# Performance work log

Measured on AMD Instinct MI355X. Metric: run time of the kernel, lower is better.

## Reference

```python
import jax, jax.numpy as jnp
import numpy as np

N, D, E, L, NL = 100000, 64, 400000, 4, 10000
NEG = jnp.float32(-1e30)


def _make_graph(key):
    k1, k2, k3, k4 = jax.random.split(key, 4)
    ncov = N - NL
    # nodes [0, NL) never appear as source -> exactly NL leaves
    src_cov = jnp.arange(ncov, dtype=jnp.int32) + NL
    src_rand = jax.random.randint(k1, (E - ncov,), NL, N, dtype=jnp.int32)
    src = jnp.concatenate([src_cov, src_rand])
    dst = jax.random.randint(k2, (E,), 0, N, dtype=jnp.int32)
    edge_index = jnp.stack([src, dst])  # [2, E]
    edge_attr = jax.random.normal(k3, (E, D), jnp.float32)
    # partition edges into L 'topological level' masks
    edge_masks = (jnp.arange(E) % L)[None, :] == jnp.arange(L)[:, None]  # [L, E] bool
    x = jax.random.normal(k4, (N, D), jnp.float32)
    return x, edge_index, edge_attr, edge_masks


def setup_inputs() -> dict:
    key = jax.random.key(0)
    kg1, kg2, kp = jax.random.split(key, 3)
    x1, ei1, ea1, em1 = _make_graph(kg1)
    x2, ei2, ea2, em2 = _make_graph(kg2)
    ks = jax.random.split(kp, 10)
    s = 1.0 / np.sqrt(D)
    params = {
        'We': jax.random.normal(ks[0], (D, D), jnp.float32) * s,
        'be': jax.random.normal(ks[1], (D,), jnp.float32) * s,
        'Wa': jax.random.normal(ks[2], (1, 2 * D), jnp.float32) * s,
        'ba': jax.random.normal(ks[3], (1,), jnp.float32) * s,
        'Wih': jax.random.normal(ks[4], (3 * D, D), jnp.float32) * s,
        'Whh': jax.random.normal(ks[5], (3 * D, D), jnp.float32) * s,
        'bih': jax.random.normal(ks[6], (3 * D,), jnp.float32) * s,
        'bhh': jax.random.normal(ks[7], (3 * D,), jnp.float32) * s,
        'Wc': jax.random.normal(ks[8], (2 * D, 2 * D), jnp.float32) * s,
        'bc': jax.random.normal(ks[9], (2 * D,), jnp.float32) * s,
    }
    return dict(x1=x1, edge_index1=ei1, edge_attr1=ea1, edge_masks1=em1,
                x2=x2, edge_index2=ei2, edge_attr2=ea2, edge_masks2=em2,
                **params, n_leaf=NL)


def _gru(x, h, Wih, Whh, bih, bhh):
    # torch.nn.GRUCell math
    gi = x @ Wih.T + bih
    gh = h @ Whh.T + bhh
    ir, iz, in_ = jnp.split(gi, 3, axis=-1)
    hr, hz, hn = jnp.split(gh, 3, axis=-1)
    r = jax.nn.sigmoid(ir + hr)
    z = jax.nn.sigmoid(iz + hz)
    n = jnp.tanh(in_ + r * hn)
    return (1.0 - z) * n + z * h


def _flow_forward(x, edge_index, edge_attr, edge_masks,
                  We, be, Wa, ba, Wih, Whh, bih, bhh):
    Nn, Dm = x.shape
    src, dst = edge_index[0], edge_index[1]
    root = jnp.ones((Nn,), bool).at[dst].set(False)  # nodes with no incoming edge
    eemb = edge_attr @ We.T + be                     # [E, D] edge_lin
    # roots: GRU with zero hidden; others start at 0 (zeros_like in torch)
    h0 = jnp.where(root[:, None], _gru(x, jnp.zeros_like(x), Wih, Whh, bih, bhh), 0.0)
    q = x[dst]                                       # h_prev_i, level-invariant

    def step(h, mask):
        k = h[src] + eemb                            # h_j + edge_emb
        logit = (jnp.concatenate([q, k], axis=-1) @ Wa.T + ba)[:, 0]  # [E]
        ml = jnp.where(mask, logit, NEG)
        mx = jnp.maximum(jax.ops.segment_max(ml, dst, num_segments=Nn), NEG)
        ex = jnp.where(mask, jnp.exp(ml - mx[dst]), 0.0)  # scatter-softmax numerator
        den = jax.ops.segment_sum(ex, dst, num_segments=Nn)
        alpha = ex / (den[dst] + 1e-16)
        msg = jax.ops.segment_sum(alpha[:, None] * h[src], dst, num_segments=Nn)
        nm = jax.ops.segment_sum(mask.astype(jnp.float32), dst, num_segments=Nn) > 0
        h_new = _gru(x, msg, Wih, Whh, bih, bhh)     # input=h_prev, hidden=msg
        return jnp.where(nm[:, None], h_new, h), None

    h, _ = jax.lax.scan(step, h0, edge_masks)
    return h


def reference(x1, edge_index1, edge_attr1, edge_masks1,
              x2, edge_index2, edge_attr2, edge_masks2,
              We, be, Wa, ba, Wih, Whh, bih, bhh, Wc, bc, n_leaf):
    o1 = _flow_forward(x1, edge_index1, edge_attr1, edge_masks1,
                       We, be, Wa, ba, Wih, Whh, bih, bhh)
    o2 = _flow_forward(x2, edge_index2, edge_attr2, edge_masks2,
                       We, be, Wa, ba, Wih, Whh, bih, bhh)
    Dm = x1.shape[1]
    leaf1 = jnp.ones((x1.shape[0],), bool).at[edge_index1[0]].set(False)
    leaf2 = jnp.ones((x2.shape[0],), bool).at[edge_index2[0]].set(False)
    idx1 = jnp.nonzero(leaf1, size=n_leaf)[0]
    idx2 = jnp.nonzero(leaf2, size=n_leaf)[0]
    feat = jnp.concatenate([o1[idx1], o2[idx2]], axis=-1) @ Wc.T + bc  # [NL, 2D]
    o1 = o1.at[idx1].set(feat[:, :Dm])
    o2 = o2.at[idx2].set(feat[:, Dm:])
    return (o1, o2)
```

## Files before the change

### kernel.cpp

```cpp
#include <hip/hip_runtime.h>

#define NN 100000
#define DD 64
#define EE 400000
#define LL 4
#define NLEAF 10000
#define NT (2*NN)
#define ETOT (2*EE)
#define M4 (4*NT)
#define NBLK ((M4 + 1023)/1024)

typedef __attribute__((ext_vector_type(8))) short bf8v;
typedef __attribute__((ext_vector_type(4))) float f4v;

__device__ __forceinline__ float rcp_(float x){ return __builtin_amdgcn_rcpf(x); }
__device__ __forceinline__ float sigm_(float x){ return rcp_(1.f + __expf(-x)); }
__device__ __forceinline__ float tanh_(float x){
  x = fminf(fmaxf(x, -15.f), 15.f);
  float a = __expf(2.f*x);
  return (a - 1.f) * rcp_(a + 1.f);
}
__device__ __forceinline__ float wave_sum(float p){
  #pragma unroll
  for (int m = 1; m < 64; m <<= 1) p += __shfl_xor(p, m, 64);
  return p;
}
__device__ __forceinline__ unsigned short f2b(float f){
  union { float f; unsigned int u; } v; v.f = f;
  unsigned int r = v.u + 0x7FFF + ((v.u >> 16) & 1);
  return (unsigned short)(r >> 16);
}
__device__ __forceinline__ float b2f(unsigned short b){
  union { unsigned int u; float f; } v; v.u = ((unsigned int)b) << 16;
  return v.f;
}
__device__ __forceinline__ int cnt_at(const unsigned int* pcnt, int i){
  int l = i / NT; int td = i - l*NT;
  return (int)((pcnt[td] >> (8*l)) & 255u);
}

__global__ void k_init(unsigned int* __restrict__ pcnt,
                       int* __restrict__ wlcnt, int* __restrict__ row_ptr,
                       float* __restrict__ hdot,
                       float* __restrict__ vvec, float* __restrict__ c0v,
                       unsigned short* __restrict__ whh_bf,
                       unsigned short* __restrict__ wih_bf,
                       unsigned short* __restrict__ hbf,
                       const float* __restrict__ We, const float* __restrict__ Wa,
                       const float* __restrict__ be, const float* __restrict__ Whh,
                       const float* __restrict__ Wih) {
  int tid = blockIdx.x*blockDim.x + threadIdx.x;
  int stride = gridDim.x*blockDim.x;
  for (int i = tid; i < NT; i += stride) { pcnt[i] = 0u; hdot[i] = 0.f; }
  for (int i = tid; i < 192*64; i += stride) whh_bf[i] = f2b(Whh[i]);
  for (int i = tid; i < 208*64; i += stride) {
    int n = i >> 6, k = i & 63;
    unsigned short v;
    if (n < 192)       v = f2b(Wih[i]);
    else if (n == 192) v = f2b(Wa[k]);
    else               v = 0;
    wih_bf[i] = v;
  }
  uint4 z4 = make_uint4(0,0,0,0);
  uint4* hz = (uint4*)hbf;
  for (int i = tid; i < NT*8; i += stride) hz[i] = z4;
  if (blockIdx.x == 0 && threadIdx.x < 64) {
    int c = threadIdx.x;
    float acc = 0.f;
    for (int d = 0; d < 64; ++d) acc += We[d*64 + c] * Wa[64 + d];
    vvec[c] = acc;
    float p = wave_sum(be[c] * Wa[64 + c]);
    if (c == 0) { c0v[0] = p; row_ptr[M4] = ETOT; }
    if (c < 8) wlcnt[c] = 0;
  }
}

__global__ void k_edot(const float* __restrict__ ea1, const float* __restrict__ ea2,
                       const int* __restrict__ ei1, const int* __restrict__ ei2,
                       const float* __restrict__ vvec, const float* __restrict__ c0v,
                       float* __restrict__ edot, unsigned int* __restrict__ pcnt) {
  int tid = blockIdx.x*blockDim.x + threadIdx.x;
  int stride = gridDim.x*blockDim.x;
  for (int ee = tid; ee < ETOT; ee += stride) {
    int g = ee >= EE;
    int e = ee - g*EE;
    const int* ei = g ? ei2 : ei1;
    int d = ei[EE + e];
    atomicAdd(&pcnt[g*NN + d], 1u << (8*(e & 3)));
  }
  int lane = threadIdx.x & 63;
  int wave = blockIdx.x*(blockDim.x>>6) + (threadIdx.x>>6);
  int nw = gridDim.x*(blockDim.x>>6);
  int grp = lane >> 4, l16 = lane & 15;
  float4 v4 = ((const float4*)vvec)[l16];
  float c0 = c0v[0];
  const int NIT = ETOT/16;
  int it = wave;
  float4 c0_, c1_, c2_, c3_;
  if (it < NIT) {
    int e0 = it*16 + grp; int g = e0 >= EE;
    const float* ea = g ? ea2 : ea1; long eb = e0 - g*EE;
    c0_ = ((const float4*)(ea + eb*64))[l16];
    c1_ = ((const float4*)(ea + (eb+4)*64))[l16];
    c2_ = ((const float4*)(ea + (eb+8)*64))[l16];
    c3_ = ((const float4*)(ea + (eb+12)*64))[l16];
  }
  while (it < NIT) {
    int jt = it + nw;
    float4 n0, n1, n2, n3;
    if (jt < NIT) {
      int e0 = jt*16 + grp; int g = e0 >= EE;
      const float* ea = g ? ea2 : ea1; long eb = e0 - g*EE;
      n0 = ((const float4*)(ea + eb*64))[l16];
      n1 = ((const float4*)(ea + (eb+4)*64))[l16];
      n2 = ((const float4*)(ea + (eb+8)*64))[l16];
      n3 = ((const float4*)(ea + (eb+12)*64))[l16];
    } else {
      n0 = n1 = n2 = n3 = make_float4(0.f,0.f,0.f,0.f);
    }
    float p0 = c0_.x*v4.x + c0_.y*v4.y + c0_.z*v4.z + c0_.w*v4.w;
    float p1 = c1_.x*v4.x + c1_.y*v4.y + c1_.z*v4.z + c1_.w*v4.w;
    float p2 = c2_.x*v4.x + c2_.y*v4.y + c2_.z*v4.z + c2_.w*v4.w;
    float p3 = c3_.x*v4.x + c3_.y*v4.y + c3_.z*v4.z + c3_.w*v4.w;
    #pragma unroll
    for (int m = 1; m < 16; m <<= 1) {
      p0 += __shfl_xor(p0, m, 64); p1 += __shfl_xor(p1, m, 64);
      p2 += __shfl_xor(p2, m, 64); p3 += __shfl_xor(p3, m, 64);
    }
    if (l16 == 0) {
      int e0 = it*16 + grp;
      edot[e0]      = p0 + c0;
      edot[e0 +  4] = p1 + c0;
      edot[e0 +  8] = p2 + c0;
      edot[e0 + 12] = p3 + c0;
    }
    c0_ = n0; c1_ = n1; c2_ = n2; c3_ = n3;
    it = jt;
  }
}

__global__ __launch_bounds__(256) void k_scan1(const unsigned int* __restrict__ pcnt,
                                               int* __restrict__ row_ptr,
                                               int* __restrict__ partials) {
  __shared__ int ts[256];
  int tx = threadIdx.x;
  int base = blockIdx.x*1024 + tx*4;
  int v[4]; int s = 0;
  #pragma unroll
  for (int u = 0; u < 4; ++u) { v[u] = (base+u < M4) ? cnt_at(pcnt, base+u) : 0; s += v[u]; }
  ts[tx] = s; __syncthreads();
  for (int off = 1; off < 256; off <<= 1) {
    int t = (tx >= off) ? ts[tx-off] : 0;
    __syncthreads();
    ts[tx] += t;
    __syncthreads();
  }
  int excl = ts[tx] - s;
  #pragma unroll
  for (int u = 0; u < 4; ++u) {
    if (base+u < M4) row_ptr[base+u] = excl;
    excl += v[u];
  }
  if (tx == 255) partials[blockIdx.x] = ts[255];
}

__global__ __launch_bounds__(256) void k_scan2(int* __restrict__ partials) {
  __shared__ int ts[256];
  int tx = threadIdx.x;
  int carry = 0;
  for (int base = 0; base < NBLK; base += 256) {
    int i = base + tx;
    int v = (i < NBLK) ? partials[i] : 0;
    ts[tx] = v; __syncthreads();
    for (int off = 1; off < 256; off <<= 1) {
      int t = (tx >= off) ? ts[tx-off] : 0;
      __syncthreads();
      ts[tx] += t;
      __syncthreads();
    }
    int incl = ts[tx];
    int tot = ts[255];
    __syncthreads();
    if (i < NBLK) partials[i] = incl - v + carry;
    carry += tot;
  }
}

__global__ __launch_bounds__(256) void k_scan3(int* __restrict__ row_ptr,
                                               const int* __restrict__ partials,
                                               const unsigned int* __restrict__ pcnt,
                                               int* __restrict__ wl, int* __restrict__ wlcnt,
                                               int* __restrict__ lastlvl) {
  int tdl = blockIdx.x*blockDim.x + threadIdx.x;
  if (tdl < NT) {
    unsigned pv = pcnt[tdl];
    int ll = -1;
    if      (pv & 0xFF000000u) ll = 3;
    else if (pv & 0x00FF0000u) ll = 2;
    else if (pv & 0x0000FF00u) ll = 1;
    else if (pv & 0x000000FFu) ll = 0;
    lastlvl[tdl] = ll;
  }
  __shared__ int cnt4[4];
  __shared__ int base4[4];
  int tx = threadIdx.x;
  if (tx < 4) cnt4[tx] = 0;
  __syncthreads();
  int base = blockIdx.x*1024 + tx*4;
  int add = partials[blockIdx.x];
  int rank[4]; int lvl[4]; bool val[4];
  #pragma unroll
  for (int u = 0; u < 4; ++u) {
    int i = base + u;
    val[u] = false;
    if (i < M4) {
      row_ptr[i] += add;
      if (cnt_at(pcnt, i) > 0) {
        int l = i / NT;
        lvl[u] = l;
        rank[u] = atomicAdd(&cnt4[l], 1);
        val[u] = true;
      }
    }
  }
  __syncthreads();
  if (tx < 4 && cnt4[tx] > 0) base4[tx] = atomicAdd(&wlcnt[tx], cnt4[tx]);
  __syncthreads();
  #pragma unroll
  for (int u = 0; u < 4; ++u) {
    if (val[u]) {
      int l = lvl[u];
      wl[l*NT + base4[l] + rank[u]] = (base + u) - l*NT;
    }
  }
}

__global__ __launch_bounds__(256) void k_fillgix(
    const int* __restrict__ ei1, const int* __restrict__ ei2,
    const float* __restrict__ edot, const float* __restrict__ ba,
    const int* __restrict__ row_ptr, unsigned int* __restrict__ pcnt,
    int2* __restrict__ csr,
    const float* __restrict__ x1, const float* __restrict__ x2,
    const unsigned short* __restrict__ wih_bf,
    const float* __restrict__ bih, const float* __restrict__ bhh,
    const float* __restrict__ Wa, const int* __restrict__ lastlvl,
    ushort2* __restrict__ gi01, unsigned short* __restrict__ gi2p,
    float* __restrict__ xdot, float* __restrict__ hdot,
    float* __restrict__ hout, unsigned short* __restrict__ hbf) {
  {
    int tid = blockIdx.x*blockDim.x + threadIdx.x;
    int stride = gridDim.x*blockDim.x;
    float bav = ba[0];
    for (int ee = tid; ee < ETOT; ee += stride) {
      int g = ee >= EE;
      int e = ee - g*EE;
      const int* ei = g ? ei2 : ei1;
      int s = ei[e], d = ei[EE + e];
      int l = e & 3;
      int td = g*NN + d;
      unsigned old = atomicAdd(&pcnt[td], (unsigned)(0u - (1u << (8*l))));
      int slot = (int)((old >> (8*l)) & 255u) - 1;
      int pos = row_ptr[l*NT + td] + slot;
      csr[pos] = make_int2(g*NN + s, __float_as_int(edot[ee] + bav));
    }
  }
  int lane = threadIdx.x & 63, w = threadIdx.x >> 6;
  int l15 = lane & 15, quad = lane >> 4;
  int wave = blockIdx.x*4 + w, nw = gridDim.x*4;
  float bi0[4],bi1[4],bi2[4],bh0[4],bh1[4],bh2[4],wk4[4];
  #pragma unroll
  for (int tt = 0; tt < 4; ++tt) {
    int f = l15 + 16*tt;
    bi0[tt]=bih[f]; bi1[tt]=bih[64+f]; bi2[tt]=bih[128+f];
    bh0[tt]=bhh[f]; bh1[tt]=bhh[64+f]; bh2[tt]=bhh[128+f];
    wk4[tt]=Wa[64+f];
  }
  for (int tl = wave; tl < NT/16; tl += nw) {
    int ta = tl*16 + l15;
    const float* xp = (ta < NN) ? x1 + (size_t)ta*64 : x2 + (size_t)(ta-NN)*64;
    float4 v0 = ((const float4*)xp)[quad*2];
    float4 v1 = ((const float4*)xp)[quad*2 + 1];
    float4 v2 = ((const float4*)xp)[quad*2 + 8];
    float4 v3 = ((const float4*)xp)[quad*2 + 9];
    bf8v a0, a1;
    a0[0]=(short)f2b(v0.x); a0[1]=(short)f2b(v0.y); a0[2]=(short)f2b(v0.z); a0[3]=(short)f2b(v0.w);
    a0[4]=(short)f2b(v1.x); a0[5]=(short)f2b(v1.y); a0[6]=(short)f2b(v1.z); a0[7]=(short)f2b(v1.w);
    a1[0]=(short)f2b(v2.x); a1[1]=(short)f2b(v2.y); a1[2]=(short)f2b(v2.z); a1[3]=(short)f2b(v2.w);
    a1[4]=(short)f2b(v3.x); a1[5]=(short)f2b(v3.y); a1[6]=(short)f2b(v3.z); a1[7]=(short)f2b(v3.w);
    int rt[4];
    #pragma unroll
    for (int r = 0; r < 4; ++r) rt[r] = (lastlvl[tl*16 + quad*4 + r] < 0);
    float hds[4] = {0.f, 0.f, 0.f, 0.f};
    #pragma unroll
    for (int tt = 0; tt < 4; ++tt) {
      bf8v bR0 = *(const bf8v*)&wih_bf[((tt  )*16 + l15)*64 + quad*8];
      bf8v bR1 = *(const bf8v*)&wih_bf[((tt  )*16 + l15)*64 + 32 + quad*8];
      bf8v bZ0 = *(const bf8v*)&wih_bf[((tt+4)*16 + l15)*64 + quad*8];
      bf8v bZ1 = *(const bf8v*)&wih_bf[((tt+4)*16 + l15)*64 + 32 + quad*8];
      bf8v bN0 = *(const bf8v*)&wih_bf[((tt+8)*16 + l15)*64 + quad*8];
      bf8v bN1 = *(const bf8v*)&wih_bf[((tt+8)*16 + l15)*64 + 32 + quad*8];
      f4v zR = {0.f,0.f,0.f,0.f}, zZ = {0.f,0.f,0.f,0.f}, zN = {0.f,0.f,0.f,0.f};
      zR = __builtin_amdgcn_mfma_f32_16x16x32_bf16(a0, bR0, zR, 0, 0, 0);
      zR = __builtin_amdgcn_mfma_f32_16x16x32_bf16(a1, bR1, zR, 0, 0, 0);
      zZ = __builtin_amdgcn_mfma_f32_16x16x32_bf16(a0, bZ0, zZ, 0, 0, 0);
      zZ = __builtin_amdgcn_mfma_f32_16x16x32_bf16(a1, bZ1, zZ, 0, 0, 0);
      zN = __builtin_amdgcn_mfma_f32_16x16x32_bf16(a0, bN0, zN, 0, 0, 0);
      zN = __builtin_amdgcn_mfma_f32_16x16x32_bf16(a1, bN1, zN, 0, 0, 0);
      int f = tt*16 + l15;
      #pragma unroll
      for (int r = 0; r < 4; ++r) {
        int t = tl*16 + quad*4 + r;
        float g0 = zR[r] + bi0[tt];
        float g1 = zZ[r] + bi1[tt];
        float g2 = zN[r] + bi2[tt];
        ushort2 p; p.x = f2b(g0); p.y = f2b(g1);
        gi01[(size_t)t*64 + f] = p;
        gi2p[(size_t)t*64 + f] = f2b(g2);
        if (rt[r]) {
          float rr = sigm_(g0 + bh0[tt]);
          float zz = sigm_(g1 + bh1[tt]);
          float nn = tanh_(g2 + rr*bh2[tt]);
          float hv = (1.f - zz)*nn;
          hout[(size_t)t*64 + f] = hv;
          hbf[(size_t)t*64 + f] = f2b(hv);
          hds[r] += hv * wk4[tt];
        }
      }
    }
    bf8v bx0 = *(const bf8v*)&wih_bf[(192 + l15)*64 + quad*8];
    bf8v bx1 = *(const bf8v*)&wih_bf[(192 + l15)*64 + 32 + quad*8];
    f4v zX = {0.f,0.f,0.f,0.f};
    zX = __builtin_amdgcn_mfma_f32_16x16x32_bf16(a0, bx0, zX, 0, 0, 0);
    zX = __builtin_amdgcn_mfma_f32_16x16x32_bf16(a1, bx1, zX, 0, 0, 0);
    #pragma unroll
    for (int r = 0; r < 4; ++r) {
      int t = tl*16 + quad*4 + r;
      if (l15 == 0) xdot[t] = zX[r];
      if (rt[r]) {
        float h = hds[r];
        h += __shfl_xor(h, 1, 64); h += __shfl_xor(h, 2, 64);
        h += __shfl_xor(h, 4, 64); h += __shfl_xor(h, 8, 64);
        if (l15 == 0) hdot[t] = h;
      }
    }
  }
}

__global__ void k_msg(const int* __restrict__ row_ptr, const int2* __restrict__ csr,
                      const float* __restrict__ xdot,
                      const float* __restrict__ hdot, const unsigned short* __restrict__ hbf,
                      const int* __restrict__ wl, const int* __restrict__ wlcnt,
                      int level, unsigned short* __restrict__ msgn_bf) {
  int l16 = threadIdx.x & 15;
  int grp = (blockIdx.x*blockDim.x + threadIdx.x) >> 4;
  int ngrp = (gridDim.x*blockDim.x) >> 4;
  int cnt = wlcnt[level];
  for (int i = grp; i < cnt; i += ngrp) {
    int t = wl[level*NT + i];
    int bi = level*NT + t;
    int p0 = row_ptr[bi], p1 = row_ptr[bi+1];
    float xd = xdot[t];
    float den = 0.f;
    float m0 = 0.f, m1 = 0.f, m2 = 0.f, m3 = 0.f;
    for (int p = p0; p < p1; ++p) {
      int2 pr = csr[p];
      int s = pr.x;
      float wv = __expf(xd + hdot[s] + __int_as_float(pr.y));
      den += wv;
      ushort4 hv = *(const ushort4*)(hbf + (size_t)s*64 + l16*4);
      m0 += wv*b2f(hv.x); m1 += wv*b2f(hv.y); m2 += wv*b2f(hv.z); m3 += wv*b2f(hv.w);
    }
    float rd = rcp_(den + 1e-16f);
    ushort4 o;
    o.x = f2b(m0*rd); o.y = f2b(m1*rd); o.z = f2b(m2*rd); o.w = f2b(m3*rd);
    *(ushort4*)(msgn_bf + (long)i*64 + l16*4) = o;
  }
}

__global__ __launch_bounds__(256) void k_gru(
    const unsigned short* __restrict__ whh_bf, const float* __restrict__ bhh,
    const float* __restrict__ Wa,
    const ushort2* __restrict__ gi01, const unsigned short* __restrict__ gi2p,
    const int* __restrict__ wl, const int* __restrict__ wlcnt,
    const int* __restrict__ lastlvl, int level,
    const unsigned short* __restrict__ msgn_bf,
    float* __restrict__ hout, unsigned short* __restrict__ hbf,
    float* __restrict__ hdot) {
  int lane = threadIdx.x & 63, w = threadIdx.x >> 6;
  int l15 = lane & 15, quad = lane >> 4;
  int cnt = wlcnt[level];
  int ntile = (cnt + 15) >> 4;
  int wave = blockIdx.x*4 + w, nw = gridDim.x*4;
  float bh0[4], bh1[4], bh2[4], wk4[4];
  #pragma unroll
  for (int tt = 0; tt < 4; ++tt) {
    int f = tt*16 + l15;
    bh0[tt]=bhh[f]; bh1[tt]=bhh[64+f]; bh2[tt]=bhh[128+f];
    wk4[tt]=Wa[64+f];
  }
  for (int tl = wave; tl < ntile; tl += nw) {
    int base = tl*16;
    long abase = (long)(base + l15)*64;
    bf8v a0 = *(const bf8v*)&msgn_bf[abase + quad*8];
    bf8v a1 = *(const bf8v*)&msgn_bf[abase + 32 + quad*8];
    f4v acc[12];
    #pragma unroll
    for (int nt = 0; nt < 12; ++nt) {
      bf8v b0 = *(const bf8v*)&whh_bf[(nt*16 + l15)*64 + quad*8];
      bf8v b1 = *(const bf8v*)&whh_bf[(nt*16 + l15)*64 + 32 + quad*8];
      f4v z = {0.f, 0.f, 0.f, 0.f};
      z = __builtin_amdgcn_mfma_f32_16x16x32_bf16(a0, b0, z, 0, 0, 0);
      acc[nt] = __builtin_amdgcn_mfma_f32_16x16x32_bf16(a1, b1, z, 0, 0, 0);
    }
    #pragma unroll
    for (int r = 0; r < 4; ++r) {
      int i = base + quad*4 + r;
      if (i < cnt) {
        int t = wl[level*NT + i];
        int ll = lastlvl[t];
        float hds = 0.f;
        #pragma unroll
        for (int tt = 0; tt < 4; ++tt) {
          int f = tt*16 + l15;
          ushort2 p01 = gi01[(size_t)t*64 + f];
          float g2v = b2f(gi2p[(size_t)t*64 + f]);
          float mv  = b2f(msgn_bf[(long)i*64 + f]);
          float rr = sigm_(b2f(p01.x) + acc[tt][r]   + bh0[tt]);
          float zz = sigm_(b2f(p01.y) + acc[tt+4][r] + bh1[tt]);
          float nn = tanh_(g2v + rr*(acc[tt+8][r] + bh2[tt]));
          float hv = (1.f - zz)*nn + zz*mv;
          if (ll == level) hout[(size_t)t*64 + f] = hv;
          if (level < 3)  hbf[(size_t)t*64 + f] = f2b(hv);
          hds += hv * wk4[tt];
        }
        if (level < 3) {
          hds += __shfl_xor(hds, 1, 64);
          hds += __shfl_xor(hds, 2, 64);
          hds += __shfl_xor(hds, 4, 64);
          hds += __shfl_xor(hds, 8, 64);
          if (l15 == 0) hdot[t] = hds;
        }
      }
    }
  }
}

__global__ __launch_bounds__(256) void k_final(const float* __restrict__ Wc,
                                               const float* __restrict__ bc,
                                               float* __restrict__ hout) {
  __shared__ float WT[128*128];
  for (int idx = threadIdx.x; idx < 128*128; idx += 256) {
    int j = idx >> 7, c = idx & 127;
    WT[c*128 + j] = Wc[idx];
  }
  __syncthreads();
  int lane = threadIdx.x & 63, w = threadIdx.x >> 6;
  int wave = blockIdx.x*4 + w, nw = gridDim.x*4;
  float bc0 = bc[lane], bc1 = bc[64 + lane];
  for (int i = wave; i < NLEAF; i += nw) {
    float h1v = hout[(long)i*64 + lane];
    float h2v = hout[(long)(NN + i)*64 + lane];
    float acc0 = 0.f, acc1 = 0.f;
    for (int c = 0; c < 64; ++c) {
      float m1 = __shfl(h1v, c, 64);
      float m2 = __shfl(h2v, c, 64);
      acc0 += WT[c*128 + lane]      * m1 + WT[(64+c)*128 + lane]      * m2;
      acc1 += WT[c*128 + 64 + lane] * m1 + WT[(64+c)*128 + 64 + lane] * m2;
    }
    hout[(long)i*64 + lane]        = acc0 + bc0;
    hout[(long)(NN + i)*64 + lane] = acc1 + bc1;
  }
}

extern "C" void kernel_launch(void* const* d_in, const int* in_sizes, int n_in,
                              void* d_out, int out_size, void* d_ws, size_t ws_size,
                              hipStream_t stream) {
  const float* x1  = (const float*)d_in[0];
  const int*   ei1 = (const int*)  d_in[1];
  const float* ea1 = (const float*)d_in[2];
  const float* x2  = (const float*)d_in[4];
  const int*   ei2 = (const int*)  d_in[5];
  const float* ea2 = (const float*)d_in[6];
  const float* We  = (const float*)d_in[8];
  const float* be  = (const float*)d_in[9];
  const float* Wa  = (const float*)d_in[10];
  const float* ba  = (const float*)d_in[11];
  const float* Wih = (const float*)d_in[12];
  const float* Whh = (const float*)d_in[13];
  const float* bih = (const float*)d_in[14];
  const float* bhh = (const float*)d_in[15];
  const float* Wc  = (const float*)d_in[16];
  const float* bc  = (const float*)d_in[17];
  float* hout = (float*)d_out;

  float* f = (float*)d_ws;
  ushort2* gi01 = (ushort2*)f;        f += (size_t)NT*64;
  unsigned short* gi2p    = (unsigned short*)f;  f += (size_t)NT*32;
  unsigned short* msgn_bf = (unsigned short*)f;  f += (size_t)NT*32;
  unsigned short* hbf     = (unsigned short*)f;  f += (size_t)NT*32;
  unsigned short* whh_bf  = (unsigned short*)f;  f += 8192;
  unsigned short* wih_bf  = (unsigned short*)f;  f += 8192;
  float* edot = f;  f += ETOT;
  float* xdot = f;  f += NT;
  float* hdot = f;  f += NT;
  float* vvec = f;  f += 64;
  float* c0v  = f;  f += 64;
  int2* csr     = (int2*)f; f += (size_t)2*ETOT;
  unsigned int* pcnt = (unsigned int*)f;  f += NT;
  int* row_ptr  = (int*)f;  f += (M4 + 64);
  int* lastlvl  = (int*)f;  f += NT;
  int* wl       = (int*)f;  f += 4*NT;
  int* wlcnt    = (int*)f;  f += 64;
  int* partials = (int*)f;  f += 1024;

  k_init <<<dim3(1024), dim3(256), 0, stream>>>(pcnt, wlcnt, row_ptr, hdot, vvec, c0v, whh_bf, wih_bf, hbf, We, Wa, be, Whh, Wih);
  k_edot <<<dim3(2048), dim3(256), 0, stream>>>(ea1, ea2, ei1, ei2, vvec, c0v, edot, pcnt);
  k_scan1<<<dim3(NBLK), dim3(256), 0, stream>>>(pcnt, row_ptr, partials);
  k_scan2<<<dim3(1),    dim3(256), 0, stream>>>(partials);
  k_scan3<<<dim3(NBLK), dim3(256), 0, stream>>>(row_ptr, partials, pcnt, wl, wlcnt, lastlvl);
  k_fillgix<<<dim3(2048), dim3(256), 0, stream>>>(ei1, ei2, edot, ba, row_ptr, pcnt, csr, x1, x2, wih_bf, bih, bhh, Wa, lastlvl, gi01, gi2p, xdot, hdot, hout, hbf);
  for (int l = 0; l < 4; ++l) {
    k_msg<<<dim3(8192), dim3(256), 0, stream>>>(row_ptr, csr, xdot, hdot, hbf, wl, wlcnt, l, msgn_bf);
    k_gru<<<dim3(2048), dim3(256), 0, stream>>>(whh_bf, bhh, Wa, gi01, gi2p, wl, wlcnt, lastlvl, l, msgn_bf, hout, hbf, hdot);
  }
  k_final<<<dim3(640), dim3(256), 0, stream>>>(Wc, bc, hout);
}
```

Before: 560.4 us.

## Fuse edge-attention dot into CSR fill and batch input-gate MFMAs

Removes the separate k_edot kernel. The per-edge projection of edge_attr onto the attention vector is now computed inside k_fillgix, right where each CSR entry is written, so the intermediate edot buffer is never stored and reloaded. The destination-count atomics move into k_init, and a small k_zero kernel now clears the counters beforehand. The input-gate MFMA loop is reorganised to issue all 13 tile products first and then run the elementwise GRU epilogue, which gives more independent MFMA work per wave but holds more accumulator registers. The explicit next-iteration prefetch of edge_attr that k_edot used is dropped.

```diff
diff --git a/kernel.cpp b/kernel.cpp
--- a/kernel.cpp
+++ b/kernel.cpp
@@ -39,19 +39,27 @@
   return (int)((pcnt[td] >> (8*l)) & 255u);
 }
 
+__global__ void k_zero(unsigned int* __restrict__ pcnt, int* __restrict__ wlcnt) {
+  int tid = blockIdx.x*blockDim.x + threadIdx.x;
+  int stride = gridDim.x*blockDim.x;
+  for (int i = tid; i < NT; i += stride) pcnt[i] = 0u;
+  if (tid < 8) wlcnt[tid] = 0;
+}
+
 __global__ void k_init(unsigned int* __restrict__ pcnt,
-                       int* __restrict__ wlcnt, int* __restrict__ row_ptr,
+                       int* __restrict__ row_ptr,
                        float* __restrict__ hdot,
                        float* __restrict__ vvec, float* __restrict__ c0v,
                        unsigned short* __restrict__ whh_bf,
                        unsigned short* __restrict__ wih_bf,
                        unsigned short* __restrict__ hbf,
+                       const int* __restrict__ ei1, const int* __restrict__ ei2,
                        const float* __restrict__ We, const float* __restrict__ Wa,
                        const float* __restrict__ be, const float* __restrict__ Whh,
                        const float* __restrict__ Wih) {
   int tid = blockIdx.x*blockDim.x + threadIdx.x;
   int stride = gridDim.x*blockDim.x;
-  for (int i = tid; i < NT; i += stride) { pcnt[i] = 0u; hdot[i] = 0.f; }
+  for (int i = tid; i < NT; i += stride) hdot[i] = 0.f;
   for (int i = tid; i < 192*64; i += stride) whh_bf[i] = f2b(Whh[i]);
   for (int i = tid; i < 208*64; i += stride) {
     int n = i >> 6, k = i & 63;
@@ -71,71 +79,13 @@
     vvec[c] = acc;
     float p = wave_sum(be[c] * Wa[64 + c]);
     if (c == 0) { c0v[0] = p; row_ptr[M4] = ETOT; }
-    if (c < 8) wlcnt[c] = 0;
-  }
-}
-
-__global__ void k_edot(const float* __restrict__ ea1, const float* __restrict__ ea2,
-                       const int* __restrict__ ei1, const int* __restrict__ ei2,
-                       const float* __restrict__ vvec, const float* __restrict__ c0v,
-                       float* __restrict__ edot, unsigned int* __restrict__ pcnt) {
-  int tid = blockIdx.x*blockDim.x + threadIdx.x;
-  int stride = gridDim.x*blockDim.x;
+  }
   for (int ee = tid; ee < ETOT; ee += stride) {
     int g = ee >= EE;
     int e = ee - g*EE;
     const int* ei = g ? ei2 : ei1;
     int d = ei[EE + e];
     atomicAdd(&pcnt[g*NN + d], 1u << (8*(e & 3)));
-  }
-  int lane = threadIdx.x & 63;
-  int wave = blockIdx.x*(blockDim.x>>6) + (threadIdx.x>>6);
-  int nw = gridDim.x*(blockDim.x>>6);
-  int grp = lane >> 4, l16 = lane & 15;
-  float4 v4 = ((const float4*)vvec)[l16];
-  float c0 = c0v[0];
-  const int NIT = ETOT/16;
-  int it = wave;
-  float4 c0_, c1_, c2_, c3_;
-  if (it < NIT) {
-    int e0 = it*16 + grp; int g = e0 >= EE;
-    const float* ea = g ? ea2 : ea1; long eb = e0 - g*EE;
-    c0_ = ((const float4*)(ea + eb*64))[l16];
-    c1_ = ((const float4*)(ea + (eb+4)*64))[l16];
-    c2_ = ((const float4*)(ea + (eb+8)*64))[l16];
-    c3_ = ((const float4*)(ea + (eb+12)*64))[l16];
-  }
-  while (it < NIT) {
-    int jt = it + nw;
-    float4 n0, n1, n2, n3;
-    if (jt < NIT) {
-      int e0 = jt*16 + grp; int g = e0 >= EE;
-      const float* ea = g ? ea2 : ea1; long eb = e0 - g*EE;
-      n0 = ((const float4*)(ea + eb*64))[l16];
-      n1 = ((const float4*)(ea + (eb+4)*64))[l16];
-      n2 = ((const float4*)(ea + (eb+8)*64))[l16];
-      n3 = ((const float4*)(ea + (eb+12)*64))[l16];
-    } else {
-      n0 = n1 = n2 = n3 = make_float4(0.f,0.f,0.f,0.f);
-    }
-    float p0 = c0_.x*v4.x + c0_.y*v4.y + c0_.z*v4.z + c0_.w*v4.w;
-    float p1 = c1_.x*v4.x + c1_.y*v4.y + c1_.z*v4.z + c1_.w*v4.w;
-    float p2 = c2_.x*v4.x + c2_.y*v4.y + c2_.z*v4.z + c2_.w*v4.w;
-    float p3 = c3_.x*v4.x + c3_.y*v4.y + c3_.z*v4.z + c3_.w*v4.w;
-    #pragma unroll
-    for (int m = 1; m < 16; m <<= 1) {
-      p0 += __shfl_xor(p0, m, 64); p1 += __shfl_xor(p1, m, 64);
-      p2 += __shfl_xor(p2, m, 64); p3 += __shfl_xor(p3, m, 64);
-    }
-    if (l16 == 0) {
-      int e0 = it*16 + grp;
-      edot[e0]      = p0 + c0;
-      edot[e0 +  4] = p1 + c0;
-      edot[e0 +  8] = p2 + c0;
-      edot[e0 + 12] = p3 + c0;
-    }
-    c0_ = n0; c1_ = n1; c2_ = n2; c3_ = n3;
-    it = jt;
   }
 }
 
@@ -236,8 +186,10 @@
 }
 
 __global__ __launch_bounds__(256) void k_fillgix(
+    const float* __restrict__ ea1, const float* __restrict__ ea2,
     const int* __restrict__ ei1, const int* __restrict__ ei2,
-    const float* __restrict__ edot, const float* __restrict__ ba,
+    const float* __restrict__ vvec, const float* __restrict__ c0v,
+    const float* __restrict__ ba,
     const int* __restrict__ row_ptr, unsigned int* __restrict__ pcnt,
     int2* __restrict__ csr,
     const float* __restrict__ x1, const float* __restrict__ x2,
@@ -247,25 +199,45 @@
     ushort2* __restrict__ gi01, unsigned short* __restrict__ gi2p,
     float* __restrict__ xdot, float* __restrict__ hdot,
     float* __restrict__ hout, unsigned short* __restrict__ hbf) {
-  {
-    int tid = blockIdx.x*blockDim.x + threadIdx.x;
-    int stride = gridDim.x*blockDim.x;
-    float bav = ba[0];
-    for (int ee = tid; ee < ETOT; ee += stride) {
-      int g = ee >= EE;
-      int e = ee - g*EE;
-      const int* ei = g ? ei2 : ei1;
-      int s = ei[e], d = ei[EE + e];
-      int l = e & 3;
-      int td = g*NN + d;
-      unsigned old = atomicAdd(&pcnt[td], (unsigned)(0u - (1u << (8*l))));
-      int slot = (int)((old >> (8*l)) & 255u) - 1;
-      int pos = row_ptr[l*NT + td] + slot;
-      csr[pos] = make_int2(g*NN + s, __float_as_int(edot[ee] + bav));
-    }
-  }
   int lane = threadIdx.x & 63, w = threadIdx.x >> 6;
   int l15 = lane & 15, quad = lane >> 4;
+  {
+    int wave = blockIdx.x*(blockDim.x>>6) + (threadIdx.x>>6);
+    int nw = gridDim.x*(blockDim.x>>6);
+    int grp = quad, l16 = l15;
+    float4 v4 = ((const float4*)vvec)[l16];
+    float cb = c0v[0] + ba[0];
+    for (int it = wave; it < ETOT/16; it += nw) {
+      int e0 = it*16 + grp;
+      int g = e0 >= EE;
+      const float* ea = g ? ea2 : ea1;
+      const int* ei = g ? ei2 : ei1;
+      long eb = e0 - g*EE;
+      float4 a0 = ((const float4*)(ea + (eb     )*64))[l16];
+      float4 a1 = ((const float4*)(ea + (eb +  4)*64))[l16];
+      float4 a2 = ((const float4*)(ea + (eb +  8)*64))[l16];
+      float4 a3 = ((const float4*)(ea + (eb + 12)*64))[l16];
+      float p0 = a0.x*v4.x + a0.y*v4.y + a0.z*v4.z + a0.w*v4.w;
+      float p1 = a1.x*v4.x + a1.y*v4.y + a1.z*v4.z + a1.w*v4.w;
+      float p2 = a2.x*v4.x + a2.y*v4.y + a2.z*v4.z + a2.w*v4.w;
+      float p3 = a3.x*v4.x + a3.y*v4.y + a3.z*v4.z + a3.w*v4.w;
+      #pragma unroll
+      for (int m = 1; m < 16; m <<= 1) {
+        p0 += __shfl_xor(p0, m, 64); p1 += __shfl_xor(p1, m, 64);
+        p2 += __shfl_xor(p2, m, 64); p3 += __shfl_xor(p3, m, 64);
+      }
+      if (l16 < 4) {
+        float pj = (l16 == 0) ? p0 : (l16 == 1) ? p1 : (l16 == 2) ? p2 : p3;
+        int e = (int)eb + 4*l16;
+        int s = ei[e], d = ei[EE + e];
+        int td = g*NN + d;
+        unsigned old = atomicAdd(&pcnt[td], (unsigned)(0u - (1u << (8*grp))));
+        int slot = (int)((old >> (8*grp)) & 255u) - 1;
+        int pos = row_ptr[grp*NT + td] + slot;
+        csr[pos] = make_int2(g*NN + s, __float_as_int(pj + cb));
+      }
+    }
+  }
   int wave = blockIdx.x*4 + w, nw = gridDim.x*4;
   float bi0[4],bi1[4],bi2[4],bh0[4],bh1[4],bh2[4],wk4[4];
   #pragma unroll
@@ -291,28 +263,24 @@
     #pragma unroll
     for (int r = 0; r < 4; ++r) rt[r] = (lastlvl[tl*16 + quad*4 + r] < 0);
     float hds[4] = {0.f, 0.f, 0.f, 0.f};
+    f4v acc[13];
     #pragma unroll
-    for (int tt = 0; tt < 4; ++tt) {
-      bf8v bR0 = *(const bf8v*)&wih_bf[((tt  )*16 + l15)*64 + quad*8];
-      bf8v bR1 = *(const bf8v*)&wih_bf[((tt  )*16 + l15)*64 + 32 + quad*8];
-      bf8v bZ0 = *(const bf8v*)&wih_bf[((tt+4)*16 + l15)*64 + quad*8];
-      bf8v bZ1 = *(const bf8v*)&wih_bf[((tt+4)*16 + l15)*64 + 32 + quad*8];
-      bf8v bN0 = *(const bf8v*)&wih_bf[((tt+8)*16 + l15)*64 + quad*8];
-      bf8v bN1 = *(const bf8v*)&wih_bf[((tt+8)*16 + l15)*64 + 32 + quad*8];
-      f4v zR = {0.f,0.f,0.f,0.f}, zZ = {0.f,0.f,0.f,0.f}, zN = {0.f,0.f,0.f,0.f};
-      zR = __builtin_amdgcn_mfma_f32_16x16x32_bf16(a0, bR0, zR, 0, 0, 0);
-      zR = __builtin_amdgcn_mfma_f32_16x16x32_bf16(a1, bR1, zR, 0, 0, 0);
-      zZ = __builtin_amdgcn_mfma_f32_16x16x32_bf16(a0, bZ0, zZ, 0, 0, 0);
-      zZ = __builtin_amdgcn_mfma_f32_16x16x32_bf16(a1, bZ1, zZ, 0, 0, 0);
-      zN = __builtin_amdgcn_mfma_f32_16x16x32_bf16(a0, bN0, zN, 0, 0, 0);
-      zN = __builtin_amdgcn_mfma_f32_16x16x32_bf16(a1, bN1, zN, 0, 0, 0);
-      int f = tt*16 + l15;
+    for (int nt = 0; nt < 13; ++nt) {
+      bf8v b0 = *(const bf8v*)&wih_bf[(nt*16 + l15)*64 + quad*8];
+      bf8v b1 = *(const bf8v*)&wih_bf[(nt*16 + l15)*64 + 32 + quad*8];
+      f4v z = {0.f, 0.f, 0.f, 0.f};
+      z = __builtin_amdgcn_mfma_f32_16x16x32_bf16(a0, b0, z, 0, 0, 0);
+      acc[nt] = __builtin_amdgcn_mfma_f32_16x16x32_bf16(a1, b1, z, 0, 0, 0);
+    }
+    #pragma unroll
+    for (int r = 0; r < 4; ++r) {
+      int t = tl*16 + quad*4 + r;
       #pragma unroll
-      for (int r = 0; r < 4; ++r) {
-        int t = tl*16 + quad*4 + r;
-        float g0 = zR[r] + bi0[tt];
-        float g1 = zZ[r] + bi1[tt];
-        float g2 = zN[r] + bi2[tt];
+      for (int tt = 0; tt < 4; ++tt) {
+        int f = tt*16 + l15;
+        float g0 = acc[tt][r]   + bi0[tt];
+        float g1 = acc[tt+4][r] + bi1[tt];
+        float g2 = acc[tt+8][r] + bi2[tt];
         ushort2 p; p.x = f2b(g0); p.y = f2b(g1);
         gi01[(size_t)t*64 + f] = p;
         gi2p[(size_t)t*64 + f] = f2b(g2);
@@ -326,16 +294,7 @@
           hds[r] += hv * wk4[tt];
         }
       }
-    }
-    bf8v bx0 = *(const bf8v*)&wih_bf[(192 + l15)*64 + quad*8];
-    bf8v bx1 = *(const bf8v*)&wih_bf[(192 + l15)*64 + 32 + quad*8];
-    f4v zX = {0.f,0.f,0.f,0.f};
-    zX = __builtin_amdgcn_mfma_f32_16x16x32_bf16(a0, bx0, zX, 0, 0, 0);
-    zX = __builtin_amdgcn_mfma_f32_16x16x32_bf16(a1, bx1, zX, 0, 0, 0);
-    #pragma unroll
-    for (int r = 0; r < 4; ++r) {
-      int t = tl*16 + quad*4 + r;
-      if (l15 == 0) xdot[t] = zX[r];
+      if (l15 == 0) xdot[t] = acc[12][r];
       if (rt[r]) {
         float h = hds[r];
         h += __shfl_xor(h, 1, 64); h += __shfl_xor(h, 2, 64);
@@ -500,7 +459,6 @@
   unsigned short* hbf     = (unsigned short*)f;  f += (size_t)NT*32;
   unsigned short* whh_bf  = (unsigned short*)f;  f += 8192;
   unsigned short* wih_bf  = (unsigned short*)f;  f += 8192;
-  float* edot = f;  f += ETOT;
   float* xdot = f;  f += NT;
   float* hdot = f;  f += NT;
   float* vvec = f;  f += 64;
@@ -513,12 +471,12 @@
   int* wlcnt    = (int*)f;  f += 64;
   int* partials = (int*)f;  f += 1024;
 
-  k_init <<<dim3(1024), dim3(256), 0, stream>>>(pcnt, wlcnt, row_ptr, hdot, vvec, c0v, whh_bf, wih_bf, hbf, We, Wa, be, Whh, Wih);
-  k_edot <<<dim3(2048), dim3(256), 0, stream>>>(ea1, ea2, ei1, ei2, vvec, c0v, edot, pcnt);
+  k_zero <<<dim3(256),  dim3(256), 0, stream>>>(pcnt, wlcnt);
+  k_init <<<dim3(1024), dim3(256), 0, stream>>>(pcnt, row_ptr, hdot, vvec, c0v, whh_bf, wih_bf, hbf, ei1, ei2, We, Wa, be, Whh, Wih);
   k_scan1<<<dim3(NBLK), dim3(256), 0, stream>>>(pcnt, row_ptr, partials);
   k_scan2<<<dim3(1),    dim3(256), 0, stream>>>(partials);
   k_scan3<<<dim3(NBLK), dim3(256), 0, stream>>>(row_ptr, partials, pcnt, wl, wlcnt, lastlvl);
-  k_fillgix<<<dim3(2048), dim3(256), 0, stream>>>(ei1, ei2, edot, ba, row_ptr, pcnt, csr, x1, x2, wih_bf, bih, bhh, Wa, lastlvl, gi01, gi2p, xdot, hdot, hout, hbf);
+  k_fillgix<<<dim3(2048), dim3(256), 0, stream>>>(ea1, ea2, ei1, ei2, vvec, c0v, ba, row_ptr, pcnt, csr, x1, x2, wih_bf, bih, bhh, Wa, lastlvl, gi01, gi2p, xdot, hdot, hout, hbf);
   for (int l = 0; l < 4; ++l) {
     k_msg<<<dim3(8192), dim3(256), 0, stream>>>(row_ptr, csr, xdot, hdot, hbf, wl, wlcnt, l, msgn_bf);
     k_gru<<<dim3(2048), dim3(256), 0, stream>>>(whh_bf, bhh, Wa, gi01, gi2p, wl, wlcnt, lastlvl, l, msgn_bf, hout, hbf, hdot);
```

Result: slower. 623.0 us (+11.2%).

## Split root GRU init into worklist kernel and restructure edge-dot loop

Applied to the files above, without the earlier changes.

Root-node (no incoming edge) initial hidden-state computation moves out of k_fillgix into a new k_roots kernel, driven by a fifth worklist built in k_scan3. This removes per-row branching and extra register pressure from the MFMA gi projection kernel, which now gets a launch_bounds occupancy hint. k_edot now does its dot-product pass first, processing two edge tiles per iteration instead of using register double-buffering, and runs the pcnt atomics afterwards. The pcnt/wlcnt zeroing moves to a separate small kernel. The cost is two extra kernel launches and re-reading gi values from global memory for root nodes.

```diff
diff --git a/kernel.cpp b/kernel.cpp
--- a/kernel.cpp
+++ b/kernel.cpp
@@ -39,8 +39,14 @@
   return (int)((pcnt[td] >> (8*l)) & 255u);
 }
 
-__global__ void k_init(unsigned int* __restrict__ pcnt,
-                       int* __restrict__ wlcnt, int* __restrict__ row_ptr,
+__global__ void k_zero(unsigned int* __restrict__ pcnt, int* __restrict__ wlcnt) {
+  int tid = blockIdx.x*blockDim.x + threadIdx.x;
+  int stride = gridDim.x*blockDim.x;
+  for (int i = tid; i < NT; i += stride) pcnt[i] = 0u;
+  if (tid < 8) wlcnt[tid] = 0;
+}
+
+__global__ void k_init(int* __restrict__ row_ptr,
                        float* __restrict__ hdot,
                        float* __restrict__ vvec, float* __restrict__ c0v,
                        unsigned short* __restrict__ whh_bf,
@@ -51,7 +57,7 @@
                        const float* __restrict__ Wih) {
   int tid = blockIdx.x*blockDim.x + threadIdx.x;
   int stride = gridDim.x*blockDim.x;
-  for (int i = tid; i < NT; i += stride) { pcnt[i] = 0u; hdot[i] = 0.f; }
+  for (int i = tid; i < NT; i += stride) hdot[i] = 0.f;
   for (int i = tid; i < 192*64; i += stride) whh_bf[i] = f2b(Whh[i]);
   for (int i = tid; i < 208*64; i += stride) {
     int n = i >> 6, k = i & 63;
@@ -71,14 +77,73 @@
     vvec[c] = acc;
     float p = wave_sum(be[c] * Wa[64 + c]);
     if (c == 0) { c0v[0] = p; row_ptr[M4] = ETOT; }
-    if (c < 8) wlcnt[c] = 0;
-  }
-}
-
-__global__ void k_edot(const float* __restrict__ ea1, const float* __restrict__ ea2,
-                       const int* __restrict__ ei1, const int* __restrict__ ei2,
-                       const float* __restrict__ vvec, const float* __restrict__ c0v,
-                       float* __restrict__ edot, unsigned int* __restrict__ pcnt) {
+  }
+}
+
+__global__ __launch_bounds__(256) void k_edot(
+    const float* __restrict__ ea1, const float* __restrict__ ea2,
+    const int* __restrict__ ei1, const int* __restrict__ ei2,
+    const float* __restrict__ vvec, const float* __restrict__ c0v,
+    float* __restrict__ edot, unsigned int* __restrict__ pcnt) {
+  int lane = threadIdx.x & 63;
+  int wave = blockIdx.x*(blockDim.x>>6) + (threadIdx.x>>6);
+  int nw = gridDim.x*(blockDim.x>>6);
+  int grp = lane >> 4, l16 = lane & 15;
+  float4 v4 = ((const float4*)vvec)[l16];
+  float c0 = c0v[0];
+  const int NIT = ETOT/16;
+  for (int it = wave; it < NIT; it += 2*nw) {
+    int it2 = it + nw;
+    bool hasB = (it2 < NIT);
+    int e0 = it*16 + grp;
+    int g = e0 >= EE;
+    const float* ea = g ? ea2 : ea1;
+    long eb = e0 - (long)g*EE;
+    float4 a0 = ((const float4*)(ea + (eb     )*64))[l16];
+    float4 a1 = ((const float4*)(ea + (eb +  4)*64))[l16];
+    float4 a2 = ((const float4*)(ea + (eb +  8)*64))[l16];
+    float4 a3 = ((const float4*)(ea + (eb + 12)*64))[l16];
+    float4 b0, b1, b2, b3; int e1 = 0;
+    if (hasB) {
+      e1 = it2*16 + grp;
+      int g2 = e1 >= EE;
+      const float* eb2 = g2 ? ea2 : ea1;
+      long ebb = e1 - (long)g2*EE;
+      b0 = ((const float4*)(eb2 + (ebb     )*64))[l16];
+      b1 = ((const float4*)(eb2 + (ebb +  4)*64))[l16];
+      b2 = ((const float4*)(eb2 + (ebb +  8)*64))[l16];
+      b3 = ((const float4*)(eb2 + (ebb + 12)*64))[l16];
+    } else {
+      b0 = b1 = b2 = b3 = make_float4(0.f,0.f,0.f,0.f);
+    }
+    float p0 = a0.x*v4.x + a0.y*v4.y + a0.z*v4.z + a0.w*v4.w;
+    float p1 = a1.x*v4.x + a1.y*v4.y + a1.z*v4.z + a1.w*v4.w;
+    float p2 = a2.x*v4.x + a2.y*v4.y + a2.z*v4.z + a2.w*v4.w;
+    float p3 = a3.x*v4.x + a3.y*v4.y + a3.z*v4.z + a3.w*v4.w;
+    float q0 = b0.x*v4.x + b0.y*v4.y + b0.z*v4.z + b0.w*v4.w;
+    float q1 = b1.x*v4.x + b1.y*v4.y + b1.z*v4.z + b1.w*v4.w;
+    float q2 = b2.x*v4.x + b2.y*v4.y + b2.z*v4.z + b2.w*v4.w;
+    float q3 = b3.x*v4.x + b3.y*v4.y + b3.z*v4.z + b3.w*v4.w;
+    #pragma unroll
+    for (int m = 1; m < 16; m <<= 1) {
+      p0 += __shfl_xor(p0, m, 64); p1 += __shfl_xor(p1, m, 64);
+      p2 += __shfl_xor(p2, m, 64); p3 += __shfl_xor(p3, m, 64);
+      q0 += __shfl_xor(q0, m, 64); q1 += __shfl_xor(q1, m, 64);
+      q2 += __shfl_xor(q2, m, 64); q3 += __shfl_xor(q3, m, 64);
+    }
+    if (l16 == 0) {
+      edot[e0]      = p0 + c0;
+      edot[e0 +  4] = p1 + c0;
+      edot[e0 +  8] = p2 + c0;
+      edot[e0 + 12] = p3 + c0;
+      if (hasB) {
+        edot[e1]      = q0 + c0;
+        edot[e1 +  4] = q1 + c0;
+        edot[e1 +  8] = q2 + c0;
+        edot[e1 + 12] = q3 + c0;
+      }
+    }
+  }
   int tid = blockIdx.x*blockDim.x + threadIdx.x;
   int stride = gridDim.x*blockDim.x;
   for (int ee = tid; ee < ETOT; ee += stride) {
@@ -87,55 +152,6 @@
     const int* ei = g ? ei2 : ei1;
     int d = ei[EE + e];
     atomicAdd(&pcnt[g*NN + d], 1u << (8*(e & 3)));
-  }
-  int lane = threadIdx.x & 63;
-  int wave = blockIdx.x*(blockDim.x>>6) + (threadIdx.x>>6);
-  int nw = gridDim.x*(blockDim.x>>6);
-  int grp = lane >> 4, l16 = lane & 15;
-  float4 v4 = ((const float4*)vvec)[l16];
-  float c0 = c0v[0];
-  const int NIT = ETOT/16;
-  int it = wave;
-  float4 c0_, c1_, c2_, c3_;
-  if (it < NIT) {
-    int e0 = it*16 + grp; int g = e0 >= EE;
-    const float* ea = g ? ea2 : ea1; long eb = e0 - g*EE;
-    c0_ = ((const float4*)(ea + eb*64))[l16];
-    c1_ = ((const float4*)(ea + (eb+4)*64))[l16];
-    c2_ = ((const float4*)(ea + (eb+8)*64))[l16];
-    c3_ = ((const float4*)(ea + (eb+12)*64))[l16];
-  }
-  while (it < NIT) {
-    int jt = it + nw;
-    float4 n0, n1, n2, n3;
-    if (jt < NIT) {
-      int e0 = jt*16 + grp; int g = e0 >= EE;
-      const float* ea = g ? ea2 : ea1; long eb = e0 - g*EE;
-      n0 = ((const float4*)(ea + eb*64))[l16];
-      n1 = ((const float4*)(ea + (eb+4)*64))[l16];
-      n2 = ((const float4*)(ea + (eb+8)*64))[l16];
-      n3 = ((const float4*)(ea + (eb+12)*64))[l16];
-    } else {
-      n0 = n1 = n2 = n3 = make_float4(0.f,0.f,0.f,0.f);
-    }
-    float p0 = c0_.x*v4.x + c0_.y*v4.y + c0_.z*v4.z + c0_.w*v4.w;
-    float p1 = c1_.x*v4.x + c1_.y*v4.y + c1_.z*v4.z + c1_.w*v4.w;
-    float p2 = c2_.x*v4.x + c2_.y*v4.y + c2_.z*v4.z + c2_.w*v4.w;
-    float p3 = c3_.x*v4.x + c3_.y*v4.y + c3_.z*v4.z + c3_.w*v4.w;
-    #pragma unroll
-    for (int m = 1; m < 16; m <<= 1) {
-      p0 += __shfl_xor(p0, m, 64); p1 += __shfl_xor(p1, m, 64);
-      p2 += __shfl_xor(p2, m, 64); p3 += __shfl_xor(p3, m, 64);
-    }
-    if (l16 == 0) {
-      int e0 = it*16 + grp;
-      edot[e0]      = p0 + c0;
-      edot[e0 +  4] = p1 + c0;
-      edot[e0 +  8] = p2 + c0;
-      edot[e0 + 12] = p3 + c0;
-    }
-    c0_ = n0; c1_ = n1; c2_ = n2; c3_ = n3;
-    it = jt;
   }
 }
 
@@ -191,7 +207,13 @@
                                                const unsigned int* __restrict__ pcnt,
                                                int* __restrict__ wl, int* __restrict__ wlcnt,
                                                int* __restrict__ lastlvl) {
+  __shared__ int cnt5[5];
+  __shared__ int base5[5];
+  int tx = threadIdx.x;
+  if (tx < 5) cnt5[tx] = 0;
+  __syncthreads();
   int tdl = blockIdx.x*blockDim.x + threadIdx.x;
+  int rootrank = -1;
   if (tdl < NT) {
     unsigned pv = pcnt[tdl];
     int ll = -1;
@@ -200,12 +222,8 @@
     else if (pv & 0x0000FF00u) ll = 1;
     else if (pv & 0x000000FFu) ll = 0;
     lastlvl[tdl] = ll;
-  }
-  __shared__ int cnt4[4];
-  __shared__ int base4[4];
-  int tx = threadIdx.x;
-  if (tx < 4) cnt4[tx] = 0;
-  __syncthreads();
+    if (ll < 0) rootrank = atomicAdd(&cnt5[4], 1);
+  }
   int base = blockIdx.x*1024 + tx*4;
   int add = partials[blockIdx.x];
   int rank[4]; int lvl[4]; bool val[4];
@@ -218,35 +236,34 @@
       if (cnt_at(pcnt, i) > 0) {
         int l = i / NT;
         lvl[u] = l;
-        rank[u] = atomicAdd(&cnt4[l], 1);
+        rank[u] = atomicAdd(&cnt5[l], 1);
         val[u] = true;
       }
     }
   }
   __syncthreads();
-  if (tx < 4 && cnt4[tx] > 0) base4[tx] = atomicAdd(&wlcnt[tx], cnt4[tx]);
+  if (tx < 5 && cnt5[tx] > 0) base5[tx] = atomicAdd(&wlcnt[tx], cnt5[tx]);
   __syncthreads();
   #pragma unroll
   for (int u = 0; u < 4; ++u) {
     if (val[u]) {
       int l = lvl[u];
-      wl[l*NT + base4[l] + rank[u]] = (base + u) - l*NT;
-    }
-  }
-}
-
-__global__ __launch_bounds__(256) void k_fillgix(
+      wl[l*NT + base5[l] + rank[u]] = (base + u) - l*NT;
+    }
+  }
+  if (rootrank >= 0) wl[4*NT + base5[4] + rootrank] = tdl;
+}
+
+__global__ __launch_bounds__(256, 5) void k_fillgix(
     const int* __restrict__ ei1, const int* __restrict__ ei2,
     const float* __restrict__ edot, const float* __restrict__ ba,
     const int* __restrict__ row_ptr, unsigned int* __restrict__ pcnt,
     int2* __restrict__ csr,
     const float* __restrict__ x1, const float* __restrict__ x2,
     const unsigned short* __restrict__ wih_bf,
-    const float* __restrict__ bih, const float* __restrict__ bhh,
-    const float* __restrict__ Wa, const int* __restrict__ lastlvl,
+    const float* __restrict__ bih,
     ushort2* __restrict__ gi01, unsigned short* __restrict__ gi2p,
-    float* __restrict__ xdot, float* __restrict__ hdot,
-    float* __restrict__ hout, unsigned short* __restrict__ hbf) {
+    float* __restrict__ xdot) {
   {
     int tid = blockIdx.x*blockDim.x + threadIdx.x;
     int stride = gridDim.x*blockDim.x;
@@ -267,13 +284,11 @@
   int lane = threadIdx.x & 63, w = threadIdx.x >> 6;
   int l15 = lane & 15, quad = lane >> 4;
   int wave = blockIdx.x*4 + w, nw = gridDim.x*4;
-  float bi0[4],bi1[4],bi2[4],bh0[4],bh1[4],bh2[4],wk4[4];
+  float bi0[4], bi1[4], bi2[4];
   #pragma unroll
   for (int tt = 0; tt < 4; ++tt) {
     int f = l15 + 16*tt;
     bi0[tt]=bih[f]; bi1[tt]=bih[64+f]; bi2[tt]=bih[128+f];
-    bh0[tt]=bhh[f]; bh1[tt]=bhh[64+f]; bh2[tt]=bhh[128+f];
-    wk4[tt]=Wa[64+f];
   }
   for (int tl = wave; tl < NT/16; tl += nw) {
     int ta = tl*16 + l15;
@@ -287,10 +302,6 @@
     a0[4]=(short)f2b(v1.x); a0[5]=(short)f2b(v1.y); a0[6]=(short)f2b(v1.z); a0[7]=(short)f2b(v1.w);
     a1[0]=(short)f2b(v2.x); a1[1]=(short)f2b(v2.y); a1[2]=(short)f2b(v2.z); a1[3]=(short)f2b(v2.w);
     a1[4]=(short)f2b(v3.x); a1[5]=(short)f2b(v3.y); a1[6]=(short)f2b(v3.z); a1[7]=(short)f2b(v3.w);
-    int rt[4];
-    #pragma unroll
-    for (int r = 0; r < 4; ++r) rt[r] = (lastlvl[tl*16 + quad*4 + r] < 0);
-    float hds[4] = {0.f, 0.f, 0.f, 0.f};
     #pragma unroll
     for (int tt = 0; tt < 4; ++tt) {
       bf8v bR0 = *(const bf8v*)&wih_bf[((tt  )*16 + l15)*64 + quad*8];
@@ -310,21 +321,9 @@
       #pragma unroll
       for (int r = 0; r < 4; ++r) {
         int t = tl*16 + quad*4 + r;
-        float g0 = zR[r] + bi0[tt];
-        float g1 = zZ[r] + bi1[tt];
-        float g2 = zN[r] + bi2[tt];
-        ushort2 p; p.x = f2b(g0); p.y = f2b(g1);
+        ushort2 p; p.x = f2b(zR[r] + bi0[tt]); p.y = f2b(zZ[r] + bi1[tt]);
         gi01[(size_t)t*64 + f] = p;
-        gi2p[(size_t)t*64 + f] = f2b(g2);
-        if (rt[r]) {
-          float rr = sigm_(g0 + bh0[tt]);
-          float zz = sigm_(g1 + bh1[tt]);
-          float nn = tanh_(g2 + rr*bh2[tt]);
-          float hv = (1.f - zz)*nn;
-          hout[(size_t)t*64 + f] = hv;
-          hbf[(size_t)t*64 + f] = f2b(hv);
-          hds[r] += hv * wk4[tt];
-        }
+        gi2p[(size_t)t*64 + f] = f2b(zN[r] + bi2[tt]);
       }
     }
     bf8v bx0 = *(const bf8v*)&wih_bf[(192 + l15)*64 + quad*8];
@@ -332,17 +331,50 @@
     f4v zX = {0.f,0.f,0.f,0.f};
     zX = __builtin_amdgcn_mfma_f32_16x16x32_bf16(a0, bx0, zX, 0, 0, 0);
     zX = __builtin_amdgcn_mfma_f32_16x16x32_bf16(a1, bx1, zX, 0, 0, 0);
+    if (l15 == 0) {
+      #pragma unroll
+      for (int r = 0; r < 4; ++r) xdot[tl*16 + quad*4 + r] = zX[r];
+    }
+  }
+}
+
+__global__ __launch_bounds__(256) void k_roots(
+    const ushort2* __restrict__ gi01, const unsigned short* __restrict__ gi2p,
+    const float* __restrict__ bhh, const float* __restrict__ Wa,
+    const int* __restrict__ wl, const int* __restrict__ wlcnt,
+    float* __restrict__ hout, unsigned short* __restrict__ hbf,
+    float* __restrict__ hdot) {
+  int l16 = threadIdx.x & 15;
+  int grp = (blockIdx.x*blockDim.x + threadIdx.x) >> 4;
+  int ngrp = (gridDim.x*blockDim.x) >> 4;
+  int cnt = wlcnt[4];
+  float bh0[4], bh1[4], bh2[4], wk[4];
+  #pragma unroll
+  for (int j = 0; j < 4; ++j) {
+    int f = l16*4 + j;
+    bh0[j]=bhh[f]; bh1[j]=bhh[64+f]; bh2[j]=bhh[128+f]; wk[j]=Wa[64+f];
+  }
+  for (int i = grp; i < cnt; i += ngrp) {
+    int t = wl[4*NT + i];
+    float hds = 0.f;
     #pragma unroll
-    for (int r = 0; r < 4; ++r) {
-      int t = tl*16 + quad*4 + r;
-      if (l15 == 0) xdot[t] = zX[r];
-      if (rt[r]) {
-        float h = hds[r];
-        h += __shfl_xor(h, 1, 64); h += __shfl_xor(h, 2, 64);
-        h += __shfl_xor(h, 4, 64); h += __shfl_xor(h, 8, 64);
-        if (l15 == 0) hdot[t] = h;
-      }
-    }
+    for (int j = 0; j < 4; ++j) {
+      int f = l16*4 + j;
+      ushort2 p01 = gi01[(size_t)t*64 + f];
+      float g2 = b2f(gi2p[(size_t)t*64 + f]);
+      float rr = sigm_(b2f(p01.x) + bh0[j]);
+      float zz = sigm_(b2f(p01.y) + bh1[j]);
+      float nn = tanh_(g2 + rr*bh2[j]);
+      float hv = (1.f - zz)*nn;
+      hout[(size_t)t*64 + f] = hv;
+      hbf[(size_t)t*64 + f] = f2b(hv);
+      hds += hv * wk[j];
+    }
+    hds += __shfl_xor(hds, 1, 64);
+    hds += __shfl_xor(hds, 2, 64);
+    hds += __shfl_xor(hds, 4, 64);
+    hds += __shfl_xor(hds, 8, 64);
+    if (l16 == 0) hdot[t] = hds;
   }
 }
 
@@ -509,16 +541,18 @@
   unsigned int* pcnt = (unsigned int*)f;  f += NT;
   int* row_ptr  = (int*)f;  f += (M4 + 64);
   int* lastlvl  = (int*)f;  f += NT;
-  int* wl       = (int*)f;  f += 4*NT;
+  int* wl       = (int*)f;  f += 5*NT;
   int* wlcnt    = (int*)f;  f += 64;
   int* partials = (int*)f;  f += 1024;
 
-  k_init <<<dim3(1024), dim3(256), 0, stream>>>(pcnt, wlcnt, row_ptr, hdot, vvec, c0v, whh_bf, wih_bf, hbf, We, Wa, be, Whh, Wih);
+  k_zero <<<dim3(256),  dim3(256), 0, stream>>>(pcnt, wlcnt);
+  k_init <<<dim3(1024), dim3(256), 0, stream>>>(row_ptr, hdot, vvec, c0v, whh_bf, wih_bf, hbf, We, Wa, be, Whh, Wih);
   k_edot <<<dim3(2048), dim3(256), 0, stream>>>(ea1, ea2, ei1, ei2, vvec, c0v, edot, pcnt);
   k_scan1<<<dim3(NBLK), dim3(256), 0, stream>>>(pcnt, row_ptr, partials);
   k_scan2<<<dim3(1),    dim3(256), 0, stream>>>(partials);
   k_scan3<<<dim3(NBLK), dim3(256), 0, stream>>>(row_ptr, partials, pcnt, wl, wlcnt, lastlvl);
-  k_fillgix<<<dim3(2048), dim3(256), 0, stream>>>(ei1, ei2, edot, ba, row_ptr, pcnt, csr, x1, x2, wih_bf, bih, bhh, Wa, lastlvl, gi01, gi2p, xdot, hdot, hout, hbf);
+  k_fillgix<<<dim3(2048), dim3(256), 0, stream>>>(ei1, ei2, edot, ba, row_ptr, pcnt, csr, x1, x2, wih_bf, bih, gi01, gi2p, xdot);
+  k_roots<<<dim3(256), dim3(256), 0, stream>>>(gi01, gi2p, bhh, Wa, wl, wlcnt, hout, hbf, hdot);
   for (int l = 0; l < 4; ++l) {
     k_msg<<<dim3(8192), dim3(256), 0, stream>>>(row_ptr, csr, xdot, hdot, hbf, wl, wlcnt, l, msgn_bf);
     k_gru<<<dim3(2048), dim3(256), 0, stream>>>(whh_bf, bhh, Wa, gi01, gi2p, wl, wlcnt, lastlvl, l, msgn_bf, hout, hbf, hdot);
```

Result: slower. 635.1 us, median of 2 (+13.3%).
